# Kernel optimization log

Hardware: AMD Instinct MI355X
Metric: run time of the kernel (lower is better)

The kernel has to match this reference:

```python
import jax, jax.numpy as jnp
import numpy as np

N_NODES = 100_000
N_EDGES = 1_600_000
F_IN = 64
H = 200
N_GRAPHS = 512
BN_EPS = 1e-5


def setup_inputs() -> dict:
    key = jax.random.key(0)
    ks = jax.random.split(key, 16)

    def w(k, shape):
        fan_in = shape[0]
        return jax.random.normal(k, shape, jnp.float32) / np.sqrt(fan_in)

    return {
        "x": jax.random.normal(ks[0], (N_NODES, F_IN), jnp.float32),
        "edge_index": jax.random.randint(ks[1], (2, N_EDGES), 0, N_NODES),
        "batch": jnp.sort(jax.random.randint(ks[2], (N_NODES,), 0, N_GRAPHS)),
        "eps1": jnp.zeros((), jnp.float32),
        "W1a": w(ks[3], (F_IN, H)), "b1a": jnp.zeros((H,), jnp.float32),
        "W1b": w(ks[4], (H, H)),    "b1b": jnp.zeros((H,), jnp.float32),
        "bn1_gamma": jnp.ones((H,), jnp.float32), "bn1_beta": jnp.zeros((H,), jnp.float32),
        "bn1_mean": 0.1 * jax.random.normal(ks[5], (H,), jnp.float32),
        "bn1_var": jax.random.uniform(ks[6], (H,), jnp.float32, 0.5, 1.5),
        "eps2": jnp.zeros((), jnp.float32),
        "W2a": w(ks[7], (H, H)), "b2a": jnp.zeros((H,), jnp.float32),
        "W2b": w(ks[8], (H, H)), "b2b": jnp.zeros((H,), jnp.float32),
        "bn2_gamma": jnp.ones((H,), jnp.float32), "bn2_beta": jnp.zeros((H,), jnp.float32),
        "bn2_mean": 0.1 * jax.random.normal(ks[9], (H,), jnp.float32),
        "bn2_var": jax.random.uniform(ks[10], (H,), jnp.float32, 0.5, 1.5),
        "Wfc": w(ks[11], (2 * H, 2)), "bfc": jnp.zeros((2,), jnp.float32),
    }


def _gin_conv(x, edge_index, eps, Wa, ba, Wb, bb):
    # GINConv: MLP((1+eps)*x + sum_{j in N(i)} x_j); messages flow src->dst
    src, dst = edge_index[0], edge_index[1]
    agg = jax.ops.segment_sum(x[src], dst, num_segments=x.shape[0])  # [N, d]
    h = (1.0 + eps) * x + agg
    return jax.nn.relu(h @ Wa + ba) @ Wb + bb


def _bn_eval(h, gamma, beta, mean, var):
    return (h - mean) * jax.lax.rsqrt(var + BN_EPS) * gamma + beta


def reference(x, edge_index, batch, eps1, W1a, b1a, W1b, b1b,
              bn1_gamma, bn1_beta, bn1_mean, bn1_var,
              eps2, W2a, b2a, W2b, b2b,
              bn2_gamma, bn2_beta, bn2_mean, bn2_var, Wfc, bfc):
    # dropout in eval mode == identity
    h = jax.nn.relu(_gin_conv(x, edge_index, eps1, W1a, b1a, W1b, b1b))
    h = _bn_eval(h, bn1_gamma, bn1_beta, bn1_mean, bn1_var)
    h = jax.nn.relu(_gin_conv(h, edge_index, eps2, W2a, b2a, W2b, b2b))
    h = _bn_eval(h, bn2_gamma, bn2_beta, bn2_mean, bn2_var)
    pooled_sum = jax.ops.segment_sum(h, batch, num_segments=N_GRAPHS)   # [G, H]
    pooled_max = jax.ops.segment_max(h, batch, num_segments=N_GRAPHS)  # [G, H]
    pooled = jnp.concatenate([pooled_sum, pooled_max], axis=1)          # [G, 2H]
    return jax.nn.log_softmax(pooled @ Wfc + bfc, axis=1)               # [G, 2]
```

## Files before the change

### kernel.cpp

```cpp
#include <hip/hip_runtime.h>
#include <hip/hip_bf16.h>
#include <math.h>

#define N_NODES 100000
#define N_EDGES 1600000
#define F_IN 64
#define H_DIM 200
#define N_GRAPHS 512
#define NB_SCAN 98

#define WT_PER (224 * 224)
#define SA 232

typedef __attribute__((ext_vector_type(8))) short short8v;
typedef __attribute__((ext_vector_type(4))) float f32x4;

__global__ void hist_kernel(const int* __restrict__ ei, int* __restrict__ cnt) {
    int i = blockIdx.x * blockDim.x + threadIdx.x;
    if (i < N_EDGES) atomicAdd(&cnt[ei[N_EDGES + i]], 1);
}

__global__ __launch_bounds__(256) void scan_part(const int* __restrict__ deg,
                                                 int* __restrict__ bsums) {
    int b = blockIdx.x, t = threadIdx.x;
    int i0 = b * 1024 + t * 4;
    int s = 0;
    #pragma unroll
    for (int k = 0; k < 4; ++k) { int i = i0 + k; if (i < N_NODES) s += deg[i]; }
    #pragma unroll
    for (int off = 32; off > 0; off >>= 1) s += __shfl_down(s, off, 64);
    __shared__ int wsum[4];
    if ((t & 63) == 0) wsum[t >> 6] = s;
    __syncthreads();
    if (t == 0) bsums[b] = wsum[0] + wsum[1] + wsum[2] + wsum[3];
}

__global__ void scan_tops(int* __restrict__ bsums, int* __restrict__ ptr) {
    __shared__ int sh[128];
    int t = threadIdx.x;
    int v = (t < NB_SCAN) ? bsums[t] : 0;
    sh[t] = v;
    __syncthreads();
    for (int off = 1; off < 128; off <<= 1) {
        int a = sh[t];
        int add = (t >= off) ? sh[t - off] : 0;
        __syncthreads();
        sh[t] = a + add;
        __syncthreads();
    }
    if (t < NB_SCAN) bsums[t] = sh[t] - v;
    if (t == 127) ptr[N_NODES] = sh[127];
}

__global__ __launch_bounds__(256) void scan_fin(int* __restrict__ deg_cursor,
                                                const int* __restrict__ bsums,
                                                int* __restrict__ ptr) {
    int b = blockIdx.x, t = threadIdx.x;
    int i0 = b * 1024 + t * 4;
    int d[4]; int s = 0;
    #pragma unroll
    for (int k = 0; k < 4; ++k) {
        int i = i0 + k;
        d[k] = (i < N_NODES) ? deg_cursor[i] : 0;
        s += d[k];
    }
    __shared__ int sh[256];
    sh[t] = s;
    __syncthreads();
    for (int off = 1; off < 256; off <<= 1) {
        int a = sh[t];
        int add = (t >= off) ? sh[t - off] : 0;
        __syncthreads();
        sh[t] = a + add;
        __syncthreads();
    }
    int run = bsums[b] + sh[t] - s;
    #pragma unroll
    for (int k = 0; k < 4; ++k) {
        int i = i0 + k;
        if (i < N_NODES) { ptr[i] = run; deg_cursor[i] = run; run += d[k]; }
    }
}

__global__ void fill_kernel(const int* __restrict__ ei, int* __restrict__ cursor,
                            int* __restrict__ csr_src) {
    int i = blockIdx.x * blockDim.x + threadIdx.x;
    if (i < N_EDGES) {
        int s = ei[i];
        int d = ei[N_EDGES + i];
        int p = atomicAdd(&cursor[d], 1);
        csr_src[p] = s;
    }
}

__device__ __forceinline__ short f2bf(float f) {
    __hip_bfloat16 h = __float2bfloat16(f);
    return *reinterpret_cast<const short*>(&h);
}
__device__ __forceinline__ float bf2f(short s) {
    return __uint_as_float(((unsigned)(unsigned short)s) << 16);
}
__device__ __forceinline__ float4 bf4_to_f4(uint2 u) {
    float4 r;
    r.x = __uint_as_float(u.x << 16);
    r.y = __uint_as_float(u.x & 0xffff0000u);
    r.z = __uint_as_float(u.y << 16);
    r.w = __uint_as_float(u.y & 0xffff0000u);
    return r;
}

__global__ void prep_w(const float* __restrict__ W1a, const float* __restrict__ W1b,
                       const float* __restrict__ W2a, const float* __restrict__ W2b,
                       short* __restrict__ wt) {
    int idx = blockIdx.x * 256 + threadIdx.x;
    if (idx >= 4 * WT_PER) return;
    int tsel = idx / WT_PER, rem = idx % WT_PER;
    int c = rem / 224, k = rem % 224;
    const float* W = (tsel == 0) ? W1a : (tsel == 1) ? W1b : (tsel == 2) ? W2a : W2b;
    int K = (tsel == 0) ? 64 : 200;
    float v = (k < K && c < 200) ? W[k * 200 + c] : 0.0f;
    short hi = f2bf(v);
    short lo = f2bf(v - bf2f(hi));
    wt[(2 * tsel) * WT_PER + rem] = hi;
    wt[(2 * tsel + 1) * WT_PER + rem] = lo;
}

template <int NKS>
__device__ __forceinline__ void gemm_split(const short* __restrict__ SLh,
                                           const short* __restrict__ SLl,
                                           const short* __restrict__ Wh,
                                           const short* __restrict__ Wl,
                                           int l15, int lhi, int rt, int ch,
                                           f32x4 acc[7]) {
    for (int ks = 0; ks < NKS; ++ks) {
        const int k0 = ks * 32 + 8 * lhi;
        short8v ah = *reinterpret_cast<const short8v*>(SLh + (rt * 16 + l15) * SA + k0);
        short8v al = *reinterpret_cast<const short8v*>(SLl + (rt * 16 + l15) * SA + k0);
        #pragma unroll
        for (int ct = 0; ct < 7; ++ct) {
            const int wrow = (ch * 7 + ct) * 16 + l15;
            short8v bh = *reinterpret_cast<const short8v*>(Wh + wrow * 224 + k0);
            short8v bl = *reinterpret_cast<const short8v*>(Wl + wrow * 224 + k0);
            acc[ct] = __builtin_amdgcn_mfma_f32_16x16x32_bf16(ah, bh, acc[ct], 0, 0, 0);
            acc[ct] = __builtin_amdgcn_mfma_f32_16x16x32_bf16(ah, bl, acc[ct], 0, 0, 0);
            acc[ct] = __builtin_amdgcn_mfma_f32_16x16x32_bf16(al, bh, acc[ct], 0, 0, 0);
        }
    }
}

template <bool FIRST>
__global__ __launch_bounds__(512, 4) void gin_mfma(
        const void* __restrict__ Xv,
        const int* __restrict__ ptr, const int* __restrict__ srcl,
        const float* __restrict__ eps_p,
        const short* __restrict__ Wa2,
        const float* __restrict__ ba,
        const short* __restrict__ Wb2, const float* __restrict__ bb,
        const float* __restrict__ gamma, const float* __restrict__ beta,
        const float* __restrict__ mean, const float* __restrict__ var,
        void* __restrict__ outv) {
    __shared__ __align__(16) short SLh[64 * SA];
    __shared__ __align__(16) short SLl[64 * SA];
    const int t = threadIdx.x;
    const int lane = t & 63;
    const int wid = t >> 6;
    const int node0 = blockIdx.x * 64;
    const float ep = 1.0f + eps_p[0];

    for (int i = t; i < 64 * 32; i += 512) {
        int row = i >> 5, c = 200 + (i & 31);
        SLh[row * SA + c] = 0;
        SLl[row * SA + c] = 0;
    }

    if (FIRST) {
        const float* X = (const float*)Xv;
        for (int rr = 0; rr < 8; ++rr) {
            int row = wid * 8 + rr;
            int node = node0 + row;
            if (node >= N_NODES) break;
            int b = ptr[node], e = ptr[node + 1];
            float a0 = ep * X[(size_t)node * 64 + lane];
            float a1 = 0.f, a2 = 0.f, a3 = 0.f, a4 = 0.f, a5 = 0.f, a6 = 0.f, a7 = 0.f;
            int j = b;
            for (; j + 8 <= e; j += 8) {
                int s0 = srcl[j+0], s1 = srcl[j+1], s2 = srcl[j+2], s3 = srcl[j+3];
                int s4 = srcl[j+4], s5 = srcl[j+5], s6 = srcl[j+6], s7 = srcl[j+7];
                a0 += X[(size_t)s0 * 64 + lane];
                a1 += X[(size_t)s1 * 64 + lane];
                a2 += X[(size_t)s2 * 64 + lane];
                a3 += X[(size_t)s3 * 64 + lane];
                a4 += X[(size_t)s4 * 64 + lane];
                a5 += X[(size_t)s5 * 64 + lane];
                a6 += X[(size_t)s6 * 64 + lane];
                a7 += X[(size_t)s7 * 64 + lane];
            }
            if (j + 4 <= e) {
                int s0 = srcl[j+0], s1 = srcl[j+1], s2 = srcl[j+2], s3 = srcl[j+3];
                a0 += X[(size_t)s0 * 64 + lane];
                a1 += X[(size_t)s1 * 64 + lane];
                a2 += X[(size_t)s2 * 64 + lane];
                a3 += X[(size_t)s3 * 64 + lane];
                j += 4;
            }
            for (; j < e; ++j) a0 += X[(size_t)srcl[j] * 64 + lane];
            float s = ((a0 + a1) + (a2 + a3)) + ((a4 + a5) + (a6 + a7));
            short hi = f2bf(s);
            SLh[row * SA + lane] = hi;
            SLl[row * SA + lane] = f2bf(s - bf2f(hi));
        }
    } else {
        const uint2* H2 = (const uint2*)Xv;
        for (int rr = 0; rr < 8; ++rr) {
            int row = wid * 8 + rr;
            int node = node0 + row;
            if (node >= N_NODES) break;
            int b = ptr[node], e = ptr[node + 1];
            if (lane < 50) {
                uint2 us = H2[(size_t)node * 50 + lane];
                float4 fs = bf4_to_f4(us);
                float4 A0 = make_float4(ep * fs.x, ep * fs.y, ep * fs.z, ep * fs.w);
                float4 A1 = make_float4(0,0,0,0), A2 = make_float4(0,0,0,0);
                float4 A3 = make_float4(0,0,0,0), A4 = make_float4(0,0,0,0);
                float4 A5 = make_float4(0,0,0,0), A6 = make_float4(0,0,0,0);
                float4 A7 = make_float4(0,0,0,0);
                int j = b;
                for (; j + 8 <= e; j += 8) {
                    int s0 = srcl[j+0], s1 = srcl[j+1], s2 = srcl[j+2], s3 = srcl[j+3];
                    int s4 = srcl[j+4], s5 = srcl[j+5], s6 = srcl[j+6], s7 = srcl[j+7];
                    float4 f0 = bf4_to_f4(H2[(size_t)s0 * 50 + lane]);
                    float4 f1 = bf4_to_f4(H2[(size_t)s1 * 50 + lane]);
                    float4 f2 = bf4_to_f4(H2[(size_t)s2 * 50 + lane]);
                    float4 f3 = bf4_to_f4(H2[(size_t)s3 * 50 + lane]);
                    float4 f4 = bf4_to_f4(H2[(size_t)s4 * 50 + lane]);
                    float4 f5 = bf4_to_f4(H2[(size_t)s5 * 50 + lane]);
                    float4 f6 = bf4_to_f4(H2[(size_t)s6 * 50 + lane]);
                    float4 f7 = bf4_to_f4(H2[(size_t)s7 * 50 + lane]);
                    A0.x += f0.x; A0.y += f0.y; A0.z += f0.z; A0.w += f0.w;
                    A1.x += f1.x; A1.y += f1.y; A1.z += f1.z; A1.w += f1.w;
                    A2.x += f2.x; A2.y += f2.y; A2.z += f2.z; A2.w += f2.w;
                    A3.x += f3.x; A3.y += f3.y; A3.z += f3.z; A3.w += f3.w;
                    A4.x += f4.x; A4.y += f4.y; A4.z += f4.z; A4.w += f4.w;
                    A5.x += f5.x; A5.y += f5.y; A5.z += f5.z; A5.w += f5.w;
                    A6.x += f6.x; A6.y += f6.y; A6.z += f6.z; A6.w += f6.w;
                    A7.x += f7.x; A7.y += f7.y; A7.z += f7.z; A7.w += f7.w;
                }
                if (j + 4 <= e) {
                    int s0 = srcl[j+0], s1 = srcl[j+1], s2 = srcl[j+2], s3 = srcl[j+3];
                    float4 f0 = bf4_to_f4(H2[(size_t)s0 * 50 + lane]);
                    float4 f1 = bf4_to_f4(H2[(size_t)s1 * 50 + lane]);
                    float4 f2 = bf4_to_f4(H2[(size_t)s2 * 50 + lane]);
                    float4 f3 = bf4_to_f4(H2[(size_t)s3 * 50 + lane]);
                    A0.x += f0.x; A0.y += f0.y; A0.z += f0.z; A0.w += f0.w;
                    A1.x += f1.x; A1.y += f1.y; A1.z += f1.z; A1.w += f1.w;
                    A2.x += f2.x; A2.y += f2.y; A2.z += f2.z; A2.w += f2.w;
                    A3.x += f3.x; A3.y += f3.y; A3.z += f3.z; A3.w += f3.w;
                    j += 4;
                }
                for (; j < e; ++j) {
                    float4 f0 = bf4_to_f4(H2[(size_t)srcl[j] * 50 + lane]);
                    A0.x += f0.x; A0.y += f0.y; A0.z += f0.z; A0.w += f0.w;
                }
                float sx = ((A0.x + A1.x) + (A2.x + A3.x)) + ((A4.x + A5.x) + (A6.x + A7.x));
                float sy = ((A0.y + A1.y) + (A2.y + A3.y)) + ((A4.y + A5.y) + (A6.y + A7.y));
                float sz = ((A0.z + A1.z) + (A2.z + A3.z)) + ((A4.z + A5.z) + (A6.z + A7.z));
                float sw = ((A0.w + A1.w) + (A2.w + A3.w)) + ((A4.w + A5.w) + (A6.w + A7.w));
                short4 ph, pl;
                ph.x = f2bf(sx); pl.x = f2bf(sx - bf2f(ph.x));
                ph.y = f2bf(sy); pl.y = f2bf(sy - bf2f(ph.y));
                ph.z = f2bf(sz); pl.z = f2bf(sz - bf2f(ph.z));
                ph.w = f2bf(sw); pl.w = f2bf(sw - bf2f(ph.w));
                *reinterpret_cast<short4*>(&SLh[row * SA + 4 * lane]) = ph;
                *reinterpret_cast<short4*>(&SLl[row * SA + 4 * lane]) = pl;
            }
        }
    }
    __syncthreads();

    const int l15 = lane & 15;
    const int lhi = lane >> 4;
    const int rt = wid >> 1;
    const int ch = wid & 1;

    f32x4 acc1[7];
    #pragma unroll
    for (int ct = 0; ct < 7; ++ct) acc1[ct] = (f32x4){0.f, 0.f, 0.f, 0.f};
    if (FIRST) gemm_split<2>(SLh, SLl, Wa2, Wa2 + WT_PER, l15, lhi, rt, ch, acc1);
    else       gemm_split<7>(SLh, SLl, Wa2, Wa2 + WT_PER, l15, lhi, rt, ch, acc1);
    __syncthreads();

    #pragma unroll
    for (int ct = 0; ct < 7; ++ct) {
        int col = (ch * 7 + ct) * 16 + l15;
        if (col < 200) {
            float bv = ba[col];
            #pragma unroll
            for (int i = 0; i < 4; ++i) {
                int row = rt * 16 + lhi * 4 + i;
                float v = fmaxf(acc1[ct][i] + bv, 0.0f);
                short hi = f2bf(v);
                SLh[row * SA + col] = hi;
                SLl[row * SA + col] = f2bf(v - bf2f(hi));
            }
        }
    }
    __syncthreads();

    f32x4 acc2[7];
    #pragma unroll
    for (int ct = 0; ct < 7; ++ct) acc2[ct] = (f32x4){0.f, 0.f, 0.f, 0.f};
    gemm_split<7>(SLh, SLl, Wb2, Wb2 + WT_PER, l15, lhi, rt, ch, acc2);

    #pragma unroll
    for (int ct = 0; ct < 7; ++ct) {
        int col = (ch * 7 + ct) * 16 + l15;
        if (col >= 200) continue;
        float bv = bb[col];
        float g0 = gamma[col], bt = beta[col], mn = mean[col];
        float inv = rsqrtf(var[col] + 1e-5f);
        #pragma unroll
        for (int i = 0; i < 4; ++i) {
            int row = rt * 16 + lhi * 4 + i;
            int node = node0 + row;
            if (node < N_NODES) {
                float v = fmaxf(acc2[ct][i] + bv, 0.0f);
                v = (v - mn) * inv * g0 + bt;
                if (FIRST) ((__hip_bfloat16*)outv)[(size_t)node * 200 + col] = __float2bfloat16(v);
                else       ((float*)outv)[(size_t)node * 200 + col] = v;
            }
        }
    }
}

__device__ __forceinline__ int lower_bound_dev(const int* a, int n, int v) {
    int lo = 0, hi = n;
    while (lo < hi) { int mid = (lo + hi) >> 1; if (a[mid] < v) lo = mid + 1; else hi = mid; }
    return lo;
}

__global__ __launch_bounds__(256) void pool_fc_kernel(const float* __restrict__ h,
        const int* __restrict__ batch, const float* __restrict__ Wfc,
        const float* __restrict__ bfc, float* __restrict__ out) {
    int g = blockIdx.x;
    __shared__ int range[2];
    if (threadIdx.x == 0) range[0] = lower_bound_dev(batch, N_NODES, g);
    else if (threadIdx.x == 64) range[1] = lower_bound_dev(batch, N_NODES, g + 1);
    __syncthreads();
    int b = range[0], e = range[1];
    int d = threadIdx.x;
    float s = 0.0f, m = -3.0e38f;
    for (int n = b; n < e; ++n) {
        if (d < 200) {
            float v = h[(size_t)n * 200 + d];
            s += v;
            m = fmaxf(m, v);
        }
    }
    float c0 = 0.f, c1 = 0.f;
    if (d < 200) {
        c0 = s * Wfc[d * 2 + 0] + m * Wfc[(200 + d) * 2 + 0];
        c1 = s * Wfc[d * 2 + 1] + m * Wfc[(200 + d) * 2 + 1];
    }
    #pragma unroll
    for (int off = 32; off > 0; off >>= 1) {
        c0 += __shfl_down(c0, off, 64);
        c1 += __shfl_down(c1, off, 64);
    }
    __shared__ float r0[4], r1[4];
    int wid = threadIdx.x >> 6;
    if ((threadIdx.x & 63) == 0) { r0[wid] = c0; r1[wid] = c1; }
    __syncthreads();
    if (threadIdx.x == 0) {
        float l0 = r0[0] + r0[1] + r0[2] + r0[3] + bfc[0];
        float l1 = r1[0] + r1[1] + r1[2] + r1[3] + bfc[1];
        float mx = fmaxf(l0, l1);
        float lse = mx + logf(expf(l0 - mx) + expf(l1 - mx));
        out[g * 2 + 0] = l0 - lse;
        out[g * 2 + 1] = l1 - lse;
    }
}

extern "C" void kernel_launch(void* const* d_in, const int* in_sizes, int n_in,
                              void* d_out, int out_size, void* d_ws, size_t ws_size,
                              hipStream_t stream) {
    const float* x    = (const float*)d_in[0];
    const int*   ei   = (const int*)d_in[1];
    const int*   batch= (const int*)d_in[2];
    const float* eps1 = (const float*)d_in[3];
    const float* W1a  = (const float*)d_in[4];
    const float* b1a  = (const float*)d_in[5];
    const float* W1b  = (const float*)d_in[6];
    const float* b1b  = (const float*)d_in[7];
    const float* bn1g = (const float*)d_in[8];
    const float* bn1b = (const float*)d_in[9];
    const float* bn1m = (const float*)d_in[10];
    const float* bn1v = (const float*)d_in[11];
    const float* eps2 = (const float*)d_in[12];
    const float* W2a  = (const float*)d_in[13];
    const float* b2a  = (const float*)d_in[14];
    const float* W2b  = (const float*)d_in[15];
    const float* b2b  = (const float*)d_in[16];
    const float* bn2g = (const float*)d_in[17];
    const float* bn2b = (const float*)d_in[18];
    const float* bn2m = (const float*)d_in[19];
    const float* bn2v = (const float*)d_in[20];
    const float* Wfc  = (const float*)d_in[21];
    const float* bfc  = (const float*)d_in[22];
    float* out = (float*)d_out;

    char* ws = (char*)d_ws;
    int* csr_ptr = (int*)(ws + 0);
    int* cursor  = (int*)(ws + 400128);
    int* csr_src = (int*)(ws + 800256);
    short* wt    = (short*)(ws + 7200256);
    short* W1a2 = wt;
    short* W1b2 = wt + 2 * WT_PER;
    short* W2a2 = wt + 4 * WT_PER;
    short* W2b2 = wt + 6 * WT_PER;
    __hip_bfloat16* h1b = (__hip_bfloat16*)(ws + 8003072);
    float* h2    = (float*)(ws + 48003072);
    int* bsums   = (int*)(ws + 8003072);

    hipMemsetAsync(cursor, 0, N_NODES * sizeof(int), stream);
    hist_kernel<<<(N_EDGES + 255) / 256, 256, 0, stream>>>(ei, cursor);
    scan_part<<<NB_SCAN, 256, 0, stream>>>(cursor, bsums);
    scan_tops<<<1, 128, 0, stream>>>(bsums, csr_ptr);
    scan_fin<<<NB_SCAN, 256, 0, stream>>>(cursor, bsums, csr_ptr);
    fill_kernel<<<(N_EDGES + 255) / 256, 256, 0, stream>>>(ei, cursor, csr_src);
    prep_w<<<(4 * WT_PER + 255) / 256, 256, 0, stream>>>(W1a, W1b, W2a, W2b, wt);

    const int NBLK = (N_NODES + 63) / 64;
    gin_mfma<true><<<NBLK, 512, 0, stream>>>(x, csr_ptr, csr_src, eps1,
            W1a2, b1a, W1b2, b1b, bn1g, bn1b, bn1m, bn1v, h1b);
    gin_mfma<false><<<NBLK, 512, 0, stream>>>(h1b, csr_ptr, csr_src, eps2,
            W2a2, b2a, W2b2, b2b, bn2g, bn2b, bn2m, bn2v, h2);

    pool_fc_kernel<<<N_GRAPHS, 256, 0, stream>>>(h2, batch, Wfc, bfc, out);
}
```

Measured before the change: 901.4 us.

## Double GIN block threads to 1024 and gather bf16 node features in layer one

Raises the GIN kernel block size from 512 to 1024 threads. Each warp now aggregates 4 rows instead of 8, and the GEMM columns are split across 4 warps per row tile (4/3/3/3 column tiles) instead of 2. A new prep_x kernel converts the input features to bf16, so the first layer's neighbor gather reads half the bytes. The unroll accumulators are cut from 8 to 4 to lower register pressure. This adds an extra conversion pass, loses precision on the layer-one inputs, and the launch bound of 8 may force register spills.

```diff
diff --git a/kernel.cpp b/kernel.cpp
--- a/kernel.cpp
+++ b/kernel.cpp
@@ -107,6 +107,11 @@
     r.z = __uint_as_float(u.y << 16);
     r.w = __uint_as_float(u.y & 0xffff0000u);
     return r;
+}
+
+__global__ void prep_x(const float* __restrict__ X, short* __restrict__ Xb) {
+    int i = blockIdx.x * 256 + threadIdx.x;
+    if (i < N_NODES * 64) Xb[i] = f2bf(X[i]);
 }
 
 __global__ void prep_w(const float* __restrict__ W1a, const float* __restrict__ W1b,
@@ -130,26 +135,28 @@
                                            const short* __restrict__ SLl,
                                            const short* __restrict__ Wh,
                                            const short* __restrict__ Wl,
-                                           int l15, int lhi, int rt, int ch,
-                                           f32x4 acc[7]) {
+                                           int l15, int lhi, int rt,
+                                           int base, int cnt, f32x4 acc[4]) {
     for (int ks = 0; ks < NKS; ++ks) {
         const int k0 = ks * 32 + 8 * lhi;
         short8v ah = *reinterpret_cast<const short8v*>(SLh + (rt * 16 + l15) * SA + k0);
         short8v al = *reinterpret_cast<const short8v*>(SLl + (rt * 16 + l15) * SA + k0);
         #pragma unroll
-        for (int ct = 0; ct < 7; ++ct) {
-            const int wrow = (ch * 7 + ct) * 16 + l15;
-            short8v bh = *reinterpret_cast<const short8v*>(Wh + wrow * 224 + k0);
-            short8v bl = *reinterpret_cast<const short8v*>(Wl + wrow * 224 + k0);
-            acc[ct] = __builtin_amdgcn_mfma_f32_16x16x32_bf16(ah, bh, acc[ct], 0, 0, 0);
-            acc[ct] = __builtin_amdgcn_mfma_f32_16x16x32_bf16(ah, bl, acc[ct], 0, 0, 0);
-            acc[ct] = __builtin_amdgcn_mfma_f32_16x16x32_bf16(al, bh, acc[ct], 0, 0, 0);
+        for (int i = 0; i < 4; ++i) {
+            if (i < cnt) {
+                const int wrow = (base + i) * 16 + l15;
+                short8v bh = *reinterpret_cast<const short8v*>(Wh + wrow * 224 + k0);
+                short8v bl = *reinterpret_cast<const short8v*>(Wl + wrow * 224 + k0);
+                acc[i] = __builtin_amdgcn_mfma_f32_16x16x32_bf16(ah, bh, acc[i], 0, 0, 0);
+                acc[i] = __builtin_amdgcn_mfma_f32_16x16x32_bf16(ah, bl, acc[i], 0, 0, 0);
+                acc[i] = __builtin_amdgcn_mfma_f32_16x16x32_bf16(al, bh, acc[i], 0, 0, 0);
+            }
         }
     }
 }
 
 template <bool FIRST>
-__global__ __launch_bounds__(512, 4) void gin_mfma(
+__global__ __launch_bounds__(1024, 8) void gin_mfma(
         const void* __restrict__ Xv,
         const int* __restrict__ ptr, const int* __restrict__ srcl,
         const float* __restrict__ eps_p,
@@ -167,83 +174,85 @@
     const int node0 = blockIdx.x * 64;
     const float ep = 1.0f + eps_p[0];
 
-    for (int i = t; i < 64 * 32; i += 512) {
+    for (int i = t; i < 64 * 32; i += 1024) {
         int row = i >> 5, c = 200 + (i & 31);
         SLh[row * SA + c] = 0;
         SLl[row * SA + c] = 0;
     }
 
     if (FIRST) {
-        const float* X = (const float*)Xv;
-        for (int rr = 0; rr < 8; ++rr) {
-            int row = wid * 8 + rr;
+        const short* Xb = (const short*)Xv;
+        for (int rr = 0; rr < 4; ++rr) {
+            int row = wid * 4 + rr;
             int node = node0 + row;
             if (node >= N_NODES) break;
             int b = ptr[node], e = ptr[node + 1];
-            float a0 = ep * X[(size_t)node * 64 + lane];
-            float a1 = 0.f, a2 = 0.f, a3 = 0.f, a4 = 0.f, a5 = 0.f, a6 = 0.f, a7 = 0.f;
+            float a0 = ep * bf2f(Xb[(size_t)node * 64 + lane]);
+            float a1 = 0.f, a2 = 0.f, a3 = 0.f;
             int j = b;
             for (; j + 8 <= e; j += 8) {
                 int s0 = srcl[j+0], s1 = srcl[j+1], s2 = srcl[j+2], s3 = srcl[j+3];
                 int s4 = srcl[j+4], s5 = srcl[j+5], s6 = srcl[j+6], s7 = srcl[j+7];
-                a0 += X[(size_t)s0 * 64 + lane];
-                a1 += X[(size_t)s1 * 64 + lane];
-                a2 += X[(size_t)s2 * 64 + lane];
-                a3 += X[(size_t)s3 * 64 + lane];
-                a4 += X[(size_t)s4 * 64 + lane];
-                a5 += X[(size_t)s5 * 64 + lane];
-                a6 += X[(size_t)s6 * 64 + lane];
-                a7 += X[(size_t)s7 * 64 + lane];
+                short f0 = Xb[(size_t)s0 * 64 + lane];
+                short f1 = Xb[(size_t)s1 * 64 + lane];
+                short f2 = Xb[(size_t)s2 * 64 + lane];
+                short f3 = Xb[(size_t)s3 * 64 + lane];
+                short f4 = Xb[(size_t)s4 * 64 + lane];
+                short f5 = Xb[(size_t)s5 * 64 + lane];
+                short f6 = Xb[(size_t)s6 * 64 + lane];
+                short f7 = Xb[(size_t)s7 * 64 + lane];
+                a0 += bf2f(f0) + bf2f(f4);
+                a1 += bf2f(f1) + bf2f(f5);
+                a2 += bf2f(f2) + bf2f(f6);
+                a3 += bf2f(f3) + bf2f(f7);
             }
             if (j + 4 <= e) {
                 int s0 = srcl[j+0], s1 = srcl[j+1], s2 = srcl[j+2], s3 = srcl[j+3];
-                a0 += X[(size_t)s0 * 64 + lane];
-                a1 += X[(size_t)s1 * 64 + lane];
-                a2 += X[(size_t)s2 * 64 + lane];
-                a3 += X[(size_t)s3 * 64 + lane];
+                a0 += bf2f(Xb[(size_t)s0 * 64 + lane]);
+                a1 += bf2f(Xb[(size_t)s1 * 64 + lane]);
+                a2 += bf2f(Xb[(size_t)s2 * 64 + lane]);
+                a3 += bf2f(Xb[(size_t)s3 * 64 + lane]);
                 j += 4;
             }
-            for (; j < e; ++j) a0 += X[(size_t)srcl[j] * 64 + lane];
-            float s = ((a0 + a1) + (a2 + a3)) + ((a4 + a5) + (a6 + a7));
+            for (; j < e; ++j) a0 += bf2f(Xb[(size_t)srcl[j] * 64 + lane]);
+            float s = (a0 + a1) + (a2 + a3);
             short hi = f2bf(s);
             SLh[row * SA + lane] = hi;
             SLl[row * SA + lane] = f2bf(s - bf2f(hi));
         }
     } else {
         const uint2* H2 = (const uint2*)Xv;
-        for (int rr = 0; rr < 8; ++rr) {
-            int row = wid * 8 + rr;
+        for (int rr = 0; rr < 4; ++rr) {
+            int row = wid * 4 + rr;
             int node = node0 + row;
             if (node >= N_NODES) break;
             int b = ptr[node], e = ptr[node + 1];
             if (lane < 50) {
-                uint2 us = H2[(size_t)node * 50 + lane];
-                float4 fs = bf4_to_f4(us);
+                float4 fs = bf4_to_f4(H2[(size_t)node * 50 + lane]);
                 float4 A0 = make_float4(ep * fs.x, ep * fs.y, ep * fs.z, ep * fs.w);
-                float4 A1 = make_float4(0,0,0,0), A2 = make_float4(0,0,0,0);
-                float4 A3 = make_float4(0,0,0,0), A4 = make_float4(0,0,0,0);
-                float4 A5 = make_float4(0,0,0,0), A6 = make_float4(0,0,0,0);
-                float4 A7 = make_float4(0,0,0,0);
+                float4 A1 = make_float4(0,0,0,0);
+                float4 A2 = make_float4(0,0,0,0);
+                float4 A3 = make_float4(0,0,0,0);
                 int j = b;
                 for (; j + 8 <= e; j += 8) {
                     int s0 = srcl[j+0], s1 = srcl[j+1], s2 = srcl[j+2], s3 = srcl[j+3];
                     int s4 = srcl[j+4], s5 = srcl[j+5], s6 = srcl[j+6], s7 = srcl[j+7];
-                    float4 f0 = bf4_to_f4(H2[(size_t)s0 * 50 + lane]);
-                    float4 f1 = bf4_to_f4(H2[(size_t)s1 * 50 + lane]);
-                    float4 f2 = bf4_to_f4(H2[(size_t)s2 * 50 + lane]);
-                    float4 f3 = bf4_to_f4(H2[(size_t)s3 * 50 + lane]);
-                    float4 f4 = bf4_to_f4(H2[(size_t)s4 * 50 + lane]);
-                    float4 f5 = bf4_to_f4(H2[(size_t)s5 * 50 + lane]);
-                    float4 f6 = bf4_to_f4(H2[(size_t)s6 * 50 + lane]);
-                    float4 f7 = bf4_to_f4(H2[(size_t)s7 * 50 + lane]);
-                    A0.x += f0.x; A0.y += f0.y; A0.z += f0.z; A0.w += f0.w;
-                    A1.x += f1.x; A1.y += f1.y; A1.z += f1.z; A1.w += f1.w;
-                    A2.x += f2.x; A2.y += f2.y; A2.z += f2.z; A2.w += f2.w;
-                    A3.x += f3.x; A3.y += f3.y; A3.z += f3.z; A3.w += f3.w;
-                    A4.x += f4.x; A4.y += f4.y; A4.z += f4.z; A4.w += f4.w;
-                    A5.x += f5.x; A5.y += f5.y; A5.z += f5.z; A5.w += f5.w;
-                    A6.x += f6.x; A6.y += f6.y; A6.z += f6.z; A6.w += f6.w;
-                    A7.x += f7.x; A7.y += f7.y; A7.z += f7.z; A7.w += f7.w;
+                    uint2 u0 = H2[(size_t)s0 * 50 + lane];
+                    uint2 u1 = H2[(size_t)s1 * 50 + lane];
+                    uint2 u2 = H2[(size_t)s2 * 50 + lane];
+                    uint2 u3 = H2[(size_t)s3 * 50 + lane];
+                    uint2 u4 = H2[(size_t)s4 * 50 + lane];
+                    uint2 u5 = H2[(size_t)s5 * 50 + lane];
+                    uint2 u6 = H2[(size_t)s6 * 50 + lane];
+                    uint2 u7 = H2[(size_t)s7 * 50 + lane];
+                    float4 f0 = bf4_to_f4(u0), f1 = bf4_to_f4(u1);
+                    float4 f2 = bf4_to_f4(u2), f3 = bf4_to_f4(u3);
+                    float4 f4 = bf4_to_f4(u4), f5 = bf4_to_f4(u5);
+                    float4 f6 = bf4_to_f4(u6), f7 = bf4_to_f4(u7);
+                    A0.x += f0.x + f4.x; A0.y += f0.y + f4.y; A0.z += f0.z + f4.z; A0.w += f0.w + f4.w;
+                    A1.x += f1.x + f5.x; A1.y += f1.y + f5.y; A1.z += f1.z + f5.z; A1.w += f1.w + f5.w;
+                    A2.x += f2.x + f6.x; A2.y += f2.y + f6.y; A2.z += f2.z + f6.z; A2.w += f2.w + f6.w;
+                    A3.x += f3.x + f7.x; A3.y += f3.y + f7.y; A3.z += f3.z + f7.z; A3.w += f3.w + f7.w;
                 }
                 if (j + 4 <= e) {
                     int s0 = srcl[j+0], s1 = srcl[j+1], s2 = srcl[j+2], s3 = srcl[j+3];
@@ -261,10 +270,10 @@
                     float4 f0 = bf4_to_f4(H2[(size_t)srcl[j] * 50 + lane]);
                     A0.x += f0.x; A0.y += f0.y; A0.z += f0.z; A0.w += f0.w;
                 }
-                float sx = ((A0.x + A1.x) + (A2.x + A3.x)) + ((A4.x + A5.x) + (A6.x + A7.x));
-                float sy = ((A0.y + A1.y) + (A2.y + A3.y)) + ((A4.y + A5.y) + (A6.y + A7.y));
-                float sz = ((A0.z + A1.z) + (A2.z + A3.z)) + ((A4.z + A5.z) + (A6.z + A7.z));
-                float sw = ((A0.w + A1.w) + (A2.w + A3.w)) + ((A4.w + A5.w) + (A6.w + A7.w));
+                float sx = (A0.x + A1.x) + (A2.x + A3.x);
+                float sy = (A0.y + A1.y) + (A2.y + A3.y);
+                float sz = (A0.z + A1.z) + (A2.z + A3.z);
+                float sw = (A0.w + A1.w) + (A2.w + A3.w);
                 short4 ph, pl;
                 ph.x = f2bf(sx); pl.x = f2bf(sx - bf2f(ph.x));
                 ph.y = f2bf(sy); pl.y = f2bf(sy - bf2f(ph.y));
@@ -279,54 +288,61 @@
 
     const int l15 = lane & 15;
     const int lhi = lane >> 4;
-    const int rt = wid >> 1;
-    const int ch = wid & 1;
-
-    f32x4 acc1[7];
-    #pragma unroll
-    for (int ct = 0; ct < 7; ++ct) acc1[ct] = (f32x4){0.f, 0.f, 0.f, 0.f};
-    if (FIRST) gemm_split<2>(SLh, SLl, Wa2, Wa2 + WT_PER, l15, lhi, rt, ch, acc1);
-    else       gemm_split<7>(SLh, SLl, Wa2, Wa2 + WT_PER, l15, lhi, rt, ch, acc1);
-    __syncthreads();
-
-    #pragma unroll
-    for (int ct = 0; ct < 7; ++ct) {
-        int col = (ch * 7 + ct) * 16 + l15;
-        if (col < 200) {
-            float bv = ba[col];
-            #pragma unroll
-            for (int i = 0; i < 4; ++i) {
-                int row = rt * 16 + lhi * 4 + i;
-                float v = fmaxf(acc1[ct][i] + bv, 0.0f);
-                short hi = f2bf(v);
-                SLh[row * SA + col] = hi;
-                SLl[row * SA + col] = f2bf(v - bf2f(hi));
-            }
-        }
-    }
-    __syncthreads();
-
-    f32x4 acc2[7];
-    #pragma unroll
-    for (int ct = 0; ct < 7; ++ct) acc2[ct] = (f32x4){0.f, 0.f, 0.f, 0.f};
-    gemm_split<7>(SLh, SLl, Wb2, Wb2 + WT_PER, l15, lhi, rt, ch, acc2);
-
-    #pragma unroll
-    for (int ct = 0; ct < 7; ++ct) {
-        int col = (ch * 7 + ct) * 16 + l15;
-        if (col >= 200) continue;
-        float bv = bb[col];
-        float g0 = gamma[col], bt = beta[col], mn = mean[col];
-        float inv = rsqrtf(var[col] + 1e-5f);
-        #pragma unroll
-        for (int i = 0; i < 4; ++i) {
-            int row = rt * 16 + lhi * 4 + i;
-            int node = node0 + row;
-            if (node < N_NODES) {
-                float v = fmaxf(acc2[ct][i] + bv, 0.0f);
-                v = (v - mn) * inv * g0 + bt;
-                if (FIRST) ((__hip_bfloat16*)outv)[(size_t)node * 200 + col] = __float2bfloat16(v);
-                else       ((float*)outv)[(size_t)node * 200 + col] = v;
+    const int rt = wid >> 2;
+    const int cq = wid & 3;
+    const int base = (cq == 0) ? 0 : (4 + 3 * (cq - 1));
+    const int cnt  = (cq == 0) ? 4 : 3;
+
+    f32x4 acc1[4];
+    #pragma unroll
+    for (int i = 0; i < 4; ++i) acc1[i] = (f32x4){0.f, 0.f, 0.f, 0.f};
+    if (FIRST) gemm_split<2>(SLh, SLl, Wa2, Wa2 + WT_PER, l15, lhi, rt, base, cnt, acc1);
+    else       gemm_split<7>(SLh, SLl, Wa2, Wa2 + WT_PER, l15, lhi, rt, base, cnt, acc1);
+    __syncthreads();
+
+    #pragma unroll
+    for (int i = 0; i < 4; ++i) {
+        if (i < cnt) {
+            int col = (base + i) * 16 + l15;
+            if (col < 200) {
+                float bv = ba[col];
+                #pragma unroll
+                for (int r = 0; r < 4; ++r) {
+                    int row = rt * 16 + lhi * 4 + r;
+                    float v = fmaxf(acc1[i][r] + bv, 0.0f);
+                    short hi = f2bf(v);
+                    SLh[row * SA + col] = hi;
+                    SLl[row * SA + col] = f2bf(v - bf2f(hi));
+                }
+            }
+        }
+    }
+    __syncthreads();
+
+    f32x4 acc2[4];
+    #pragma unroll
+    for (int i = 0; i < 4; ++i) acc2[i] = (f32x4){0.f, 0.f, 0.f, 0.f};
+    gemm_split<7>(SLh, SLl, Wb2, Wb2 + WT_PER, l15, lhi, rt, base, cnt, acc2);
+
+    #pragma unroll
+    for (int i = 0; i < 4; ++i) {
+        if (i < cnt) {
+            int col = (base + i) * 16 + l15;
+            if (col < 200) {
+                float bv = bb[col];
+                float g0 = gamma[col], bt = beta[col], mn = mean[col];
+                float inv = rsqrtf(var[col] + 1e-5f);
+                #pragma unroll
+                for (int r = 0; r < 4; ++r) {
+                    int row = rt * 16 + lhi * 4 + r;
+                    int node = node0 + row;
+                    if (node < N_NODES) {
+                        float v = fmaxf(acc2[i][r] + bv, 0.0f);
+                        v = (v - mn) * inv * g0 + bt;
+                        if (FIRST) ((__hip_bfloat16*)outv)[(size_t)node * 200 + col] = __float2bfloat16(v);
+                        else       ((float*)outv)[(size_t)node * 200 + col] = v;
+                    }
+                }
             }
         }
     }
@@ -417,9 +433,10 @@
     short* W1b2 = wt + 2 * WT_PER;
     short* W2a2 = wt + 4 * WT_PER;
     short* W2b2 = wt + 6 * WT_PER;
-    __hip_bfloat16* h1b = (__hip_bfloat16*)(ws + 8003072);
-    float* h2    = (float*)(ws + 48003072);
-    int* bsums   = (int*)(ws + 8003072);
+    short* Xb    = (short*)(ws + 8003072);
+    __hip_bfloat16* h1b = (__hip_bfloat16*)(ws + 20803072);
+    float* h2    = (float*)(ws + 60803072);
+    int* bsums   = (int*)(ws + 20803072);
 
     hipMemsetAsync(cursor, 0, N_NODES * sizeof(int), stream);
     hist_kernel<<<(N_EDGES + 255) / 256, 256, 0, stream>>>(ei, cursor);
@@ -428,11 +445,12 @@
     scan_fin<<<NB_SCAN, 256, 0, stream>>>(cursor, bsums, csr_ptr);
     fill_kernel<<<(N_EDGES + 255) / 256, 256, 0, stream>>>(ei, cursor, csr_src);
     prep_w<<<(4 * WT_PER + 255) / 256, 256, 0, stream>>>(W1a, W1b, W2a, W2b, wt);
+    prep_x<<<(N_NODES * 64 + 255) / 256, 256, 0, stream>>>(x, Xb);
 
     const int NBLK = (N_NODES + 63) / 64;
-    gin_mfma<true><<<NBLK, 512, 0, stream>>>(x, csr_ptr, csr_src, eps1,
+    gin_mfma<true><<<NBLK, 1024, 0, stream>>>(Xb, csr_ptr, csr_src, eps1,
             W1a2, b1a, W1b2, b1b, bn1g, bn1b, bn1m, bn1v, h1b);
-    gin_mfma<false><<<NBLK, 512, 0, stream>>>(h1b, csr_ptr, csr_src, eps2,
+    gin_mfma<false><<<NBLK, 1024, 0, stream>>>(h1b, csr_ptr, csr_src, eps2,
             W2a2, b2a, W2b2, b2b, bn2g, bn2b, bn2m, bn2v, h2);
 
     pool_fc_kernel<<<N_GRAPHS, 256, 0, stream>>>(h2, batch, Wfc, bfc, out);
```

Measured after the change: 924.9 us. +2.6%, slower.
